# Kernel tuning notes

Measured on AMD Instinct MI355X. Metric: run time of the kernel, lower is better.

## Reference

```python
import jax, jax.numpy as jnp
import numpy as np

N, C, S = 262144, 256, 16
BN_EPS = 1e-5


def setup_inputs() -> dict:
    key = jax.random.key(0)
    ks = jax.random.split(key, 8)
    x = jax.random.normal(ks[0], (N, C), dtype=jnp.float32)
    # strictly increasing cumulative offsets ending at N (guarantees nonzero counts)
    rng = np.random.default_rng(0)
    cuts = np.sort(rng.choice(np.arange(1, N), size=S - 1, replace=False))
    o = jnp.asarray(np.concatenate([cuts, [N]]), dtype=jnp.int64)
    # linear2_: Linear(C, C) (+ReLU, no BN in this branch)
    W2 = jax.random.normal(ks[1], (C, C), dtype=jnp.float32) / np.sqrt(C)
    b2 = jax.random.normal(ks[2], (C,), dtype=jnp.float32) * 0.01
    # linear1_: Linear(2C, C) + BatchNorm1d(C) + ReLU
    W1 = jax.random.normal(ks[3], (2 * C, C), dtype=jnp.float32) / np.sqrt(2 * C)
    b1 = jax.random.normal(ks[4], (C,), dtype=jnp.float32) * 0.01
    gamma = jnp.ones((C,), dtype=jnp.float32)
    beta = jnp.zeros((C,), dtype=jnp.float32)
    run_mean = jax.random.normal(ks[5], (C,), dtype=jnp.float32) * 0.01
    run_var = jnp.ones((C,), dtype=jnp.float32)
    return {"x": x, "o": o, "W2": W2, "b2": b2, "W1": W1, "b1": b1,
            "gamma": gamma, "beta": beta, "run_mean": run_mean, "run_var": run_var}


def reference(x, o, W2, b2, W1, b1, gamma, beta, run_mean, run_var):
    n, c = x.shape
    num_seg = o.shape[0]
    # segment id of each point: first offset strictly greater than index
    seg_ids = jnp.searchsorted(o, jnp.arange(n), side="right")  # [N]
    counts = jnp.diff(o, prepend=0).astype(x.dtype)             # [S]
    sums = jax.ops.segment_sum(x, seg_ids, num_segments=num_seg)  # [S, C]
    means = sums / counts[:, None]
    # linear2_ on per-segment mean, broadcast back to points
    h = jax.nn.relu(means @ W2 + b2)                            # [S, C]
    xc = jnp.concatenate([x, h[seg_ids]], axis=1)               # [N, 2C]
    # linear1_: Linear + BatchNorm1d (inference, running stats) + ReLU
    y = xc @ W1 + b1
    y = (y - run_mean) * jax.lax.rsqrt(run_var + BN_EPS) * gamma + beta
    return jax.nn.relu(y)
```

## Files before the change

kernel.cpp:

```cpp
#include <hip/hip_runtime.h>

#define C_DIM 256
#define S_SEG 16
#define N_PTS 262144

typedef __attribute__((ext_vector_type(8))) short bf16x8;
typedef __attribute__((ext_vector_type(4))) short bf16x4;
typedef __attribute__((ext_vector_type(4))) float f32x4;

__device__ __forceinline__ short f2bf(float f) {
    unsigned u = __builtin_bit_cast(unsigned, f);
    u += 0x7FFF + ((u >> 16) & 1);
    return (short)(u >> 16);
}

__device__ __forceinline__ int o_get(const int* __restrict__ o_raw, int i) {
    return (o_raw[1] == 0) ? o_raw[2 * i] : o_raw[i];
}

template <bool WRITE_XB>
__global__ __launch_bounds__(256) void k1_segsum(const float* __restrict__ x,
                                                 const int* __restrict__ o_raw,
                                                 float* __restrict__ sums,
                                                 short* __restrict__ xb) {
    __shared__ int o_s[S_SEG];
    __shared__ float4 partv[256];
    __shared__ int pseg[256];
    int t = threadIdx.x;
    if (t < S_SEG) o_s[t] = o_get(o_raw, t);
    __syncthreads();

    int rsub = t >> 6, cg = t & 63;
    int row0 = blockIdx.x * 256 + rsub * 64;
    const float4* xv = (const float4*)x;

    int cur = 0;
#pragma unroll
    for (int j = 0; j < S_SEG; ++j) cur += (row0 >= o_s[j]);
    int next = o_s[cur];

    float4 acc = make_float4(0.f, 0.f, 0.f, 0.f);
    for (int i = 0; i < 64; ++i) {
        int row = row0 + i;
        if (row >= next) {
            atomicAdd(&sums[cur * C_DIM + cg * 4 + 0], acc.x);
            atomicAdd(&sums[cur * C_DIM + cg * 4 + 1], acc.y);
            atomicAdd(&sums[cur * C_DIM + cg * 4 + 2], acc.z);
            atomicAdd(&sums[cur * C_DIM + cg * 4 + 3], acc.w);
            acc = make_float4(0.f, 0.f, 0.f, 0.f);
            do { cur++; next = o_s[cur]; } while (row >= next);
        }
        float4 v = xv[row * 64 + cg];
        if (WRITE_XB) {
            bf16x4 w;
            w[0] = f2bf(v.x); w[1] = f2bf(v.y); w[2] = f2bf(v.z); w[3] = f2bf(v.w);
            *(bf16x4*)&xb[(row << 8) + (cg << 2)] = w;
        }
        acc.x += v.x; acc.y += v.y; acc.z += v.z; acc.w += v.w;
    }
    partv[t] = acc;
    pseg[t] = cur;
    __syncthreads();

    if (t < 64) {
        float4 a = partv[t];
        int s = pseg[t];
        for (int i = 1; i < 4; ++i) {
            int idx = i * 64 + t;
            int s2 = pseg[idx];
            float4 a2 = partv[idx];
            if (s2 == s) {
                a.x += a2.x; a.y += a2.y; a.z += a2.z; a.w += a2.w;
            } else {
                atomicAdd(&sums[s * C_DIM + t * 4 + 0], a.x);
                atomicAdd(&sums[s * C_DIM + t * 4 + 1], a.y);
                atomicAdd(&sums[s * C_DIM + t * 4 + 2], a.z);
                atomicAdd(&sums[s * C_DIM + t * 4 + 3], a.w);
                s = s2; a = a2;
            }
        }
        atomicAdd(&sums[s * C_DIM + t * 4 + 0], a.x);
        atomicAdd(&sums[s * C_DIM + t * 4 + 1], a.y);
        atomicAdd(&sums[s * C_DIM + t * 4 + 2], a.z);
        atomicAdd(&sums[s * C_DIM + t * 4 + 3], a.w);
    }
}

__global__ __launch_bounds__(256) void k2_small(const float* __restrict__ sums,
                                                const int* __restrict__ o_raw,
                                                const float* __restrict__ W2,
                                                const float* __restrict__ b2,
                                                const float* __restrict__ W1,
                                                const float* __restrict__ b1,
                                                const float* __restrict__ gamma,
                                                const float* __restrict__ beta,
                                                const float* __restrict__ rmean,
                                                const float* __restrict__ rvar,
                                                float* __restrict__ Cseg,
                                                short* __restrict__ W1s) {
    int t = threadIdx.x;
    int blk = blockIdx.x;
    if (blk < S_SEG) {
        __shared__ float mean_s[C_DIM];
        __shared__ float h_s[C_DIM];
        int s = blk;
        int lo = (s == 0) ? 0 : o_get(o_raw, s - 1);
        float inv = 1.0f / (float)(o_get(o_raw, s) - lo);
        mean_s[t] = sums[s * C_DIM + t] * inv;
        __syncthreads();
        float acc = b2[t];
#pragma unroll 4
        for (int k = 0; k < C_DIM; ++k) acc = fmaf(mean_s[k], W2[k * C_DIM + t], acc);
        h_s[t] = fmaxf(acc, 0.0f);
        __syncthreads();
        float acc2 = 0.f;
#pragma unroll 4
        for (int k = 0; k < C_DIM; ++k) acc2 = fmaf(h_s[k], W1[(C_DIM + k) * C_DIM + t], acc2);
        float sc = gamma[t] * rsqrtf(rvar[t] + 1e-5f);
        Cseg[s * C_DIM + t] = (b1[t] + acc2 - rmean[t]) * sc + beta[t];
    } else {
        int base = (blk - S_SEG) * 8192;
        for (int i = 0; i < 32; ++i) {
            int idx = base + i * 256 + t;
            int k = idx >> 8, c = idx & 255;
            float sc = gamma[c] * rsqrtf(rvar[c] + 1e-5f);
            float v = W1[k * C_DIM + c] * sc;
            int kb2 = k >> 5, q = (k >> 3) & 3, j = k & 7, nsub = c >> 4, r = c & 15;
            int off = ((kb2 * 16 + nsub) * 64 + q * 16 + r) * 8 + j;
            W1s[off] = f2bf(v);
        }
    }
}

#define K3_LOAD(A, B, kb)                                                          \
    {                                                                              \
        _Pragma("unroll")                                                          \
        for (int kt = 0; kt < 2; ++kt) {                                           \
            _Pragma("unroll")                                                      \
            for (int mt = 0; mt < 4; ++mt)                                         \
                A[kt][mt] = *(const bf16x8*)&xb[abase[mt] + (kb) * 64 + kt * 32];  \
            _Pragma("unroll")                                                      \
            for (int nt = 0; nt < 4; ++nt)                                         \
                B[kt][nt] = *(const bf16x8*)&W1s[(kb) * 16384 + kt * 8192 + bb + nt * 512]; \
        }                                                                          \
    }

#define K3_MFMA(A, B)                                                              \
    {                                                                              \
        _Pragma("unroll")                                                          \
        for (int kt = 0; kt < 2; ++kt)                                             \
            _Pragma("unroll")                                                      \
            for (int mt = 0; mt < 4; ++mt)                                         \
                _Pragma("unroll")                                                  \
                for (int nt = 0; nt < 4; ++nt)                                     \
                    acc[mt][nt] = __builtin_amdgcn_mfma_f32_16x16x32_bf16(          \
                        A[kt][mt], B[kt][nt], acc[mt][nt], 0, 0, 0);               \
    }

__global__ __launch_bounds__(256) void k3_gemm(const short* __restrict__ xb,
                                               const short* __restrict__ W1s,
                                               const float* __restrict__ Cseg,
                                               const int* __restrict__ o_raw,
                                               float* __restrict__ out) {
    int t = threadIdx.x;
    int wave = t >> 6, lane = t & 63;
    int q = lane >> 4, r = lane & 15;
    int m0 = (int)blockIdx.x * 64;

    f32x4 acc[4][4];
#pragma unroll
    for (int mt = 0; mt < 4; ++mt)
#pragma unroll
        for (int nt = 0; nt < 4; ++nt)
            acc[mt][nt] = (f32x4){0.f, 0.f, 0.f, 0.f};

    int abase[4];
#pragma unroll
    for (int mt = 0; mt < 4; ++mt) abase[mt] = ((m0 + mt * 16 + r) << 8) + (q << 3);
    int bb = (wave << 11) + (lane << 3);

    bf16x8 a0[2][4], b0[2][4], a1[2][4], b1[2][4];
    K3_LOAD(a0, b0, 0)
    K3_LOAD(a1, b1, 1)
    K3_MFMA(a0, b0)
    K3_LOAD(a0, b0, 2)
    K3_MFMA(a1, b1)
    K3_LOAD(a1, b1, 3)
    K3_MFMA(a0, b0)
    K3_MFMA(a1, b1)

    int ov[S_SEG];
#pragma unroll
    for (int j = 0; j < S_SEG; ++j) ov[j] = o_get(o_raw, j);

#pragma unroll
    for (int mt = 0; mt < 4; ++mt) {
#pragma unroll
        for (int i = 0; i < 4; ++i) {
            int row = m0 + mt * 16 + q * 4 + i;
            int s = 0;
#pragma unroll
            for (int j = 0; j < S_SEG; ++j) s += (row >= ov[j]);
#pragma unroll
            for (int nt = 0; nt < 4; ++nt) {
                int col = wave * 64 + nt * 16 + r;
                float v = acc[mt][nt][i] + Cseg[s * C_DIM + col];
                __builtin_nontemporal_store(fmaxf(v, 0.0f), &out[(long)row * C_DIM + col]);
            }
        }
    }
}

__global__ __launch_bounds__(256) void k3_gemm_f32lds(const float* __restrict__ x,
                                                      const short* __restrict__ W1s,
                                                      const float* __restrict__ Cseg,
                                                      const int* __restrict__ o_raw,
                                                      float* __restrict__ out) {
    __shared__ __align__(16) short As[2][4 * 2 * 64 * 8];
    __shared__ int o_s[S_SEG];

    int t = threadIdx.x;
    int wave = t >> 6, lane = t & 63;
    int q = lane >> 4, r = lane & 15;
    int wc = wave;
    int m0 = (int)(gridDim.x - 1 - blockIdx.x) * 64;

    if (t < S_SEG) o_s[t] = o_get(o_raw, t);

    f32x4 acc[4][4];
#pragma unroll
    for (int mt = 0; mt < 4; ++mt)
#pragma unroll
        for (int nt = 0; nt < 4; ++nt)
            acc[mt][nt] = (f32x4){0.f, 0.f, 0.f, 0.f};

    const float4* xv = (const float4*)x;
    int arow = t >> 3;
    int akc = t & 7;
    int kt_w = akc >> 2, q_w = akc & 3;
    int mt0 = arow >> 4, r0 = arow & 15;
    int slot0 = (mt0 * 2 + kt_w) * 64 + q_w * 16 + (r0 ^ q_w);
    int row1 = 32 + arow, mt1 = row1 >> 4, r1 = row1 & 15;
    int slot1 = (mt1 * 2 + kt_w) * 64 + q_w * 16 + (r1 ^ q_w);
    long gbase0 = (long)(m0 + arow) * 64 + akc * 2;
    long gbase1 = (long)(m0 + 32 + arow) * 64 + akc * 2;

    float4 c00, c01, c10, c11;
    c00 = xv[gbase0]; c01 = xv[gbase0 + 1];
    c10 = xv[gbase1]; c11 = xv[gbase1 + 1];
    {
        bf16x8 w0, w1;
        w0[0] = f2bf(c00.x); w0[1] = f2bf(c00.y); w0[2] = f2bf(c00.z); w0[3] = f2bf(c00.w);
        w0[4] = f2bf(c01.x); w0[5] = f2bf(c01.y); w0[6] = f2bf(c01.z); w0[7] = f2bf(c01.w);
        *(bf16x8*)&As[0][slot0 * 8] = w0;
        w1[0] = f2bf(c10.x); w1[1] = f2bf(c10.y); w1[2] = f2bf(c10.z); w1[3] = f2bf(c10.w);
        w1[4] = f2bf(c11.x); w1[5] = f2bf(c11.y); w1[6] = f2bf(c11.z); w1[7] = f2bf(c11.w);
        *(bf16x8*)&As[0][slot1 * 8] = w1;
    }
    __syncthreads();

    for (int kb = 0; kb < 4; ++kb) {
        if (kb < 3) {
            long o = (long)(kb + 1) * 16;
            c00 = xv[gbase0 + o]; c01 = xv[gbase0 + o + 1];
            c10 = xv[gbase1 + o]; c11 = xv[gbase1 + o + 1];
        }
        const short* Ab = As[kb & 1];
#pragma unroll
        for (int kt = 0; kt < 2; ++kt) {
            bf16x8 a[4], b[4];
#pragma unroll
            for (int mt = 0; mt < 4; ++mt)
                a[mt] = *(const bf16x8*)&Ab[((mt * 2 + kt) * 64 + q * 16 + (r ^ q)) * 8];
#pragma unroll
            for (int nt = 0; nt < 4; ++nt)
                b[nt] = *(const bf16x8*)&W1s[(((kb * 2 + kt) * 16 + wc * 4 + nt) * 64 + lane) * 8];
#pragma unroll
            for (int mt = 0; mt < 4; ++mt)
#pragma unroll
                for (int nt = 0; nt < 4; ++nt)
                    acc[mt][nt] = __builtin_amdgcn_mfma_f32_16x16x32_bf16(a[mt], b[nt], acc[mt][nt], 0, 0, 0);
        }
        if (kb < 3) {
            short* Aw = As[(kb + 1) & 1];
            bf16x8 w0, w1;
            w0[0] = f2bf(c00.x); w0[1] = f2bf(c00.y); w0[2] = f2bf(c00.z); w0[3] = f2bf(c00.w);
            w0[4] = f2bf(c01.x); w0[5] = f2bf(c01.y); w0[6] = f2bf(c01.z); w0[7] = f2bf(c01.w);
            *(bf16x8*)&Aw[slot0 * 8] = w0;
            w1[0] = f2bf(c10.x); w1[1] = f2bf(c10.y); w1[2] = f2bf(c10.z); w1[3] = f2bf(c10.w);
            w1[4] = f2bf(c11.x); w1[5] = f2bf(c11.y); w1[6] = f2bf(c11.z); w1[7] = f2bf(c11.w);
            *(bf16x8*)&Aw[slot1 * 8] = w1;
            __syncthreads();
        }
    }

#pragma unroll
    for (int mt = 0; mt < 4; ++mt) {
#pragma unroll
        for (int i = 0; i < 4; ++i) {
            int row = m0 + mt * 16 + q * 4 + i;
            int s = 0;
#pragma unroll
            for (int j = 0; j < S_SEG; ++j) s += (row >= o_s[j]);
#pragma unroll
            for (int nt = 0; nt < 4; ++nt) {
                int col = wc * 64 + nt * 16 + r;
                float v = acc[mt][nt][i] + Cseg[s * C_DIM + col];
                __builtin_nontemporal_store(fmaxf(v, 0.0f), &out[(long)row * C_DIM + col]);
            }
        }
    }
}

extern "C" void kernel_launch(void* const* d_in, const int* in_sizes, int n_in,
                              void* d_out, int out_size, void* d_ws, size_t ws_size,
                              hipStream_t stream) {
    const float* x     = (const float*)d_in[0];
    const int*   o     = (const int*)d_in[1];
    const float* W2    = (const float*)d_in[2];
    const float* b2    = (const float*)d_in[3];
    const float* W1    = (const float*)d_in[4];
    const float* b1    = (const float*)d_in[5];
    const float* gamma = (const float*)d_in[6];
    const float* beta  = (const float*)d_in[7];
    const float* rmean = (const float*)d_in[8];
    const float* rvar  = (const float*)d_in[9];
    float* out = (float*)d_out;

    const int N = N_PTS;

    float* sums = (float*)d_ws;
    float* Cseg = (float*)((char*)d_ws + 16384);
    short* W1s  = (short*)((char*)d_ws + 65536);
    size_t xb_off = (size_t)1 << 20;
    short* xb   = (short*)((char*)d_ws + xb_off);
    size_t need = xb_off + (size_t)N * C_DIM * 2;

    hipMemsetAsync(d_ws, 0, 16384, stream);
    if (ws_size >= need) {
        k1_segsum<true><<<N / 256, 256, 0, stream>>>(x, o, sums, xb);
        k2_small<<<24, 256, 0, stream>>>(sums, o, W2, b2, W1, b1, gamma, beta, rmean, rvar, Cseg, W1s);
        k3_gemm<<<N / 64, 256, 0, stream>>>(xb, W1s, Cseg, o, out);
    } else {
        k1_segsum<false><<<N / 256, 256, 0, stream>>>(x, o, sums, nullptr);
        k2_small<<<24, 256, 0, stream>>>(sums, o, W2, b2, W1, b1, gamma, beta, rmean, rvar, Cseg, W1s);
        k3_gemm_f32lds<<<N / 64, 256, 0, stream>>>(x, W1s, Cseg, o, out);
    }
}
```

Measured before the change: 645.0 us.

## Stage GEMM A tiles via direct global-to-LDS loads with swizzle and double buffering

The bf16 GEMM kernel now copies its A-operand (xb rows) into a double-buffered, XOR-swizzled LDS tile with global_load_lds instead of loading it per lane into registers. Blocks are also walked in reverse order, and segment offsets sit in shared memory. Separately, the segment-sum kernel halves rows per block and doubles the grid to raise parallelism. The aim is lower VGPR pressure and better latency hiding in the GEMM, paid for with extra barriers and LDS traffic, plus more atomics in k1.

```diff
diff --git a/kernel.cpp b/kernel.cpp
--- a/kernel.cpp
+++ b/kernel.cpp
@@ -16,6 +16,12 @@
 
 __device__ __forceinline__ int o_get(const int* __restrict__ o_raw, int i) {
     return (o_raw[1] == 0) ? o_raw[2 * i] : o_raw[i];
+}
+
+typedef const unsigned int __attribute__((address_space(1)))* gas_ptr;
+typedef unsigned int __attribute__((address_space(3)))* las_ptr;
+__device__ __forceinline__ void gl_lds16(const void* g, void* l) {
+    __builtin_amdgcn_global_load_lds((gas_ptr)g, (las_ptr)l, 16, 0, 0);
 }
 
 template <bool WRITE_XB>
@@ -31,7 +37,7 @@
     __syncthreads();
 
     int rsub = t >> 6, cg = t & 63;
-    int row0 = blockIdx.x * 256 + rsub * 64;
+    int row0 = blockIdx.x * 128 + rsub * 32;
     const float4* xv = (const float4*)x;
 
     int cur = 0;
@@ -40,7 +46,7 @@
     int next = o_s[cur];
 
     float4 acc = make_float4(0.f, 0.f, 0.f, 0.f);
-    for (int i = 0; i < 64; ++i) {
+    for (int i = 0; i < 32; ++i) {
         int row = row0 + i;
         if (row >= next) {
             atomicAdd(&sums[cur * C_DIM + cg * 4 + 0], acc.x);
@@ -132,40 +138,20 @@
     }
 }
 
-#define K3_LOAD(A, B, kb)                                                          \
-    {                                                                              \
-        _Pragma("unroll")                                                          \
-        for (int kt = 0; kt < 2; ++kt) {                                           \
-            _Pragma("unroll")                                                      \
-            for (int mt = 0; mt < 4; ++mt)                                         \
-                A[kt][mt] = *(const bf16x8*)&xb[abase[mt] + (kb) * 64 + kt * 32];  \
-            _Pragma("unroll")                                                      \
-            for (int nt = 0; nt < 4; ++nt)                                         \
-                B[kt][nt] = *(const bf16x8*)&W1s[(kb) * 16384 + kt * 8192 + bb + nt * 512]; \
-        }                                                                          \
-    }
-
-#define K3_MFMA(A, B)                                                              \
-    {                                                                              \
-        _Pragma("unroll")                                                          \
-        for (int kt = 0; kt < 2; ++kt)                                             \
-            _Pragma("unroll")                                                      \
-            for (int mt = 0; mt < 4; ++mt)                                         \
-                _Pragma("unroll")                                                  \
-                for (int nt = 0; nt < 4; ++nt)                                     \
-                    acc[mt][nt] = __builtin_amdgcn_mfma_f32_16x16x32_bf16(          \
-                        A[kt][mt], B[kt][nt], acc[mt][nt], 0, 0, 0);               \
-    }
-
 __global__ __launch_bounds__(256) void k3_gemm(const short* __restrict__ xb,
                                                const short* __restrict__ W1s,
                                                const float* __restrict__ Cseg,
                                                const int* __restrict__ o_raw,
                                                float* __restrict__ out) {
+    __shared__ __align__(16) char AsB[2][8192];
+    __shared__ int o_s[S_SEG];
+
     int t = threadIdx.x;
     int wave = t >> 6, lane = t & 63;
     int q = lane >> 4, r = lane & 15;
-    int m0 = (int)blockIdx.x * 64;
+    int m0 = (int)(gridDim.x - 1 - blockIdx.x) * 64;
+
+    if (t < S_SEG) o_s[t] = o_get(o_raw, t);
 
     f32x4 acc[4][4];
 #pragma unroll
@@ -174,24 +160,43 @@
         for (int nt = 0; nt < 4; ++nt)
             acc[mt][nt] = (f32x4){0.f, 0.f, 0.f, 0.f};
 
-    int abase[4];
-#pragma unroll
-    for (int mt = 0; mt < 4; ++mt) abase[mt] = ((m0 + mt * 16 + r) << 8) + (q << 3);
-    int bb = (wave << 11) + (lane << 3);
-
-    bf16x8 a0[2][4], b0[2][4], a1[2][4], b1[2][4];
-    K3_LOAD(a0, b0, 0)
-    K3_LOAD(a1, b1, 1)
-    K3_MFMA(a0, b0)
-    K3_LOAD(a0, b0, 2)
-    K3_MFMA(a1, b1)
-    K3_LOAD(a1, b1, 3)
-    K3_MFMA(a0, b0)
-    K3_MFMA(a1, b1)
-
-    int ov[S_SEG];
-#pragma unroll
-    for (int j = 0; j < S_SEG; ++j) ov[j] = o_get(o_raw, j);
+    int s0 = wave * 128 + lane;
+    int s1 = s0 + 64;
+    int mk0 = s0 >> 6, u0 = s0 & 63, q0 = u0 >> 4, r0 = (u0 & 15) ^ q0;
+    int mk1 = s1 >> 6, u1 = s1 & 63, q1 = u1 >> 4, r1 = (u1 & 15) ^ q1;
+    long src0 = (long)((mk0 >> 1) * 16 + r0) * 512 + (mk0 & 1) * 64 + q0 * 16;
+    long src1 = (long)((mk1 >> 1) * 16 + r1) * 512 + (mk1 & 1) * 64 + q1 * 16;
+    const char* xbB = (const char*)xb + (long)m0 * 512;
+    int ldsu0 = (wave * 128) * 16;
+    int ldsu1 = (wave * 128 + 64) * 16;
+
+#define K3_STAGE(bi, kb)                                        \
+    gl_lds16(xbB + src0 + (kb) * 128, &AsB[bi][ldsu0]);         \
+    gl_lds16(xbB + src1 + (kb) * 128, &AsB[bi][ldsu1]);
+
+    K3_STAGE(0, 0)
+    __syncthreads();
+
+    for (int kb = 0; kb < 4; ++kb) {
+        if (kb < 3) { K3_STAGE((kb + 1) & 1, kb + 1) }
+        const short* Ab = (const short*)AsB[kb & 1];
+#pragma unroll
+        for (int kt = 0; kt < 2; ++kt) {
+            bf16x8 a[4], b[4];
+#pragma unroll
+            for (int mt = 0; mt < 4; ++mt)
+                a[mt] = *(const bf16x8*)&Ab[((mt * 2 + kt) * 64 + q * 16 + (r ^ q)) * 8];
+#pragma unroll
+            for (int nt = 0; nt < 4; ++nt)
+                b[nt] = *(const bf16x8*)&W1s[(((kb * 2 + kt) * 16 + wave * 4 + nt) * 64 + lane) * 8];
+#pragma unroll
+            for (int mt = 0; mt < 4; ++mt)
+#pragma unroll
+                for (int nt = 0; nt < 4; ++nt)
+                    acc[mt][nt] = __builtin_amdgcn_mfma_f32_16x16x32_bf16(a[mt], b[nt], acc[mt][nt], 0, 0, 0);
+        }
+        if (kb < 3) __syncthreads();
+    }
 
 #pragma unroll
     for (int mt = 0; mt < 4; ++mt) {
@@ -200,7 +205,7 @@
             int row = m0 + mt * 16 + q * 4 + i;
             int s = 0;
 #pragma unroll
-            for (int j = 0; j < S_SEG; ++j) s += (row >= ov[j]);
+            for (int j = 0; j < S_SEG; ++j) s += (row >= o_s[j]);
 #pragma unroll
             for (int nt = 0; nt < 4; ++nt) {
                 int col = wave * 64 + nt * 16 + r;
@@ -209,6 +214,7 @@
             }
         }
     }
+#undef K3_STAGE
 }
 
 __global__ __launch_bounds__(256) void k3_gemm_f32lds(const float* __restrict__ x,
@@ -338,11 +344,11 @@
 
     hipMemsetAsync(d_ws, 0, 16384, stream);
     if (ws_size >= need) {
-        k1_segsum<true><<<N / 256, 256, 0, stream>>>(x, o, sums, xb);
+        k1_segsum<true><<<N / 128, 256, 0, stream>>>(x, o, sums, xb);
         k2_small<<<24, 256, 0, stream>>>(sums, o, W2, b2, W1, b1, gamma, beta, rmean, rvar, Cseg, W1s);
         k3_gemm<<<N / 64, 256, 0, stream>>>(xb, W1s, Cseg, o, out);
     } else {
-        k1_segsum<false><<<N / 256, 256, 0, stream>>>(x, o, sums, nullptr);
+        k1_segsum<false><<<N / 128, 256, 0, stream>>>(x, o, sums, nullptr);
         k2_small<<<24, 256, 0, stream>>>(sums, o, W2, b2, W1, b1, gamma, beta, rmean, rvar, Cseg, W1s);
         k3_gemm_f32lds<<<N / 64, 256, 0, stream>>>(x, W1s, Cseg, o, out);
     }
```

Measured after the change: 638.4 us. About the same (-1.0%).
